# Performance work log

Measured on AMD Instinct MI355X. Metric: run time of the kernel, lower is better.

## Reference

```python
import jax, jax.numpy as jnp
import numpy as np

N, T, D, H = 100000, 16, 8, 40
HP1 = H + 1
ALPHA_DP = 1.0
KAPPA0 = 1000.0   # priorGaussianVarKappa
NU0 = 100.0       # priorWishartNu
PSI0_SCALE = 500.0  # priorWishartPsi = 500*I


def setup_inputs() -> dict:
    key = jax.random.key(0)
    ks = jax.random.split(key, 6)
    return {
        "BetaGamma1": jnp.ones((1, T), jnp.float32),
        "Phi": jax.random.uniform(ks[0], (N, T), jnp.float32),
        "inputData": jax.random.normal(ks[1], (N, D), jnp.float32),
        "outputData": jax.random.normal(ks[2], (N, 1), jnp.float32),
        "weightELM": jax.random.uniform(ks[3], (D, H), jnp.float32) * 2.0 - 1.0,
        "biasELM": jax.random.normal(ks[4], (H, 1), jnp.float32),
        "epsilonA": jnp.ones((1, T), jnp.float32),
        "epsilonB": jnp.ones((1, T), jnp.float32),
        "zetaA": 1e-4 * jnp.ones((1, T), jnp.float32),
        "zetaB": jnp.ones((1, T), jnp.float32),
    }


def reference(BetaGamma1, Phi, inputData, outputData, weightELM, biasELM,
              epsilonA, epsilonB, zetaA, zetaB):
    f32 = jnp.float32
    mu0 = jnp.zeros((D, 1), f32)                      # priorGaussianMeanMu
    Psi0 = PSI0_SCALE * jnp.eye(D, dtype=f32)         # priorWishartPsi

    sumPhi = jnp.sum(Phi, axis=0, keepdims=True)      # [1,T]

    # stick-breaking Beta params. Torch builds a flipped [T,N,T] tril mask;
    # mathematically BetaGamma2[t] = alpha + sum_{j>t} sum_n Phi[n,j]
    BetaGamma1_new = jnp.ones_like(BetaGamma1) + sumPhi
    col = sumPhi[0]                                   # [T]
    rev_incl = jnp.cumsum(col[::-1])[::-1]            # sum_{j>=t}
    BetaGamma2 = (ALPHA_DP + (rev_incl - col))[None, :]

    # Gaussian-Wishart natural-parameter updates.
    # Torch loops over clusters doing [N,D,D] bmm outer products; this is
    # S[:,:,t] = sum_n Phi[n,t] x_n x_n^T
    S = jnp.einsum('nt,ni,nj->ijt', Phi, inputData, inputData)  # [D,D,T]
    t11 = -0.5 * (Psi0 + KAPPA0 * mu0 @ mu0.T)[:, :, None] - 0.5 * S
    t12 = KAPPA0 * mu0 + inputData.T @ Phi            # [D,T]
    t21 = -0.5 * sumPhi - 0.5 * (NU0 + D + 2)         # [1,T]
    kappa = KAPPA0 + sumPhi                           # [1,T]
    mu = t12 / kappa                                  # [D,T]
    nu = -2.0 * t21 - 2.0 - float(D)                  # [1,T]
    psi = -2.0 * t11 - kappa[0][None, None, :] * jnp.einsum('it,jt->ijt', mu, mu)

    # ELM feature map + augmented design matrix X = [sigmoid(x W + b), 1]
    hmap = jax.nn.sigmoid(inputData @ weightELM + biasELM.T)   # [N,H]
    X = jnp.concatenate([hmap, jnp.ones((inputData.shape[0], 1), f32)], axis=1)  # [N,HP1]

    epsExp = (epsilonA / epsilonB)[0]                 # [T]
    zetaExp = (zetaA / zetaB)[0]                      # [T]

    # A[t] = X^T diag(Phi[:,t]) X   (torch: per-cluster bmm with diag_embed)
    A = jnp.einsum('nt,ni,nj->tij', Phi, X, X)        # [T,HP1,HP1]
    WS = jnp.linalg.inv(epsExp[:, None, None] * A
                        + zetaExp[:, None, None] * jnp.eye(HP1, dtype=f32))
    # b[t] = X^T diag(Phi[:,t]) y
    b = jnp.einsum('ni,nt->ti', X * outputData, Phi)  # [T,HP1]
    WMv = zetaExp[:, None] * jnp.einsum('tij,tj->ti', WS, b)   # [T,HP1]
    WM = WMv[:, :, None]                              # [T,HP1,1]

    # prior Zeta/Epsilon alias the variational initial values in __init__
    zetaA_new = zetaA + (H + 1) * 0.5
    zetaB_new = zetaB + 0.5 * (jnp.sum(WMv * WMv, axis=1)
                               + jnp.trace(WS, axis1=-2, axis2=-1))[None, :]
    epsA_new = epsilonA + 0.5 * sumPhi

    pred = jnp.einsum('ni,ti->tn', X, WMv)            # [T,N]
    err = outputData.T - pred                          # [T,N]
    t1 = jnp.einsum('tn,nt->t', err * err, Phi)[None, :]
    t2 = jnp.einsum('tij,tji->t', A, WS)[None, :]
    epsB_new = epsilonB + 0.5 * (t1 + t2)

    return (BetaGamma1_new, BetaGamma2, mu, kappa, nu, psi,
            WM, WS, zetaA_new, zetaB_new, epsA_new, epsB_new)
```

## Files before the change

kernel.cpp:

```cpp
#include <hip/hip_runtime.h>

#define Nn 100000
#define Tt 16
#define Dd 8
#define Hh 40
#define HP1 41

#define SPC 13
#define CH  (32 * SPC)
#define KCMAX ((Nn + CH - 1) / CH)

#define CSZ 53248
#define XEH_OFF  0
#define XEL_OFF  (XEH_OFF + 32 * Nn)
#define PHIT_OFF (XEL_OFF + 32 * Nn)
#define PART_OFF (PHIT_OFF + 16 * Nn)
#define P_OFF    (PART_OFF + 8 * CSZ)

#define OFF_BG1   0
#define OFF_BG2   16
#define OFF_MU    32
#define OFF_KAPPA 160
#define OFF_NU    176
#define OFF_PSI   192
#define OFF_WM    1216
#define OFF_WS    1872
#define OFF_ZA    28768
#define OFF_ZB    28784
#define OFF_EA    28800
#define OFF_EB    28816

typedef _Float16 f16x8 __attribute__((ext_vector_type(8)));
typedef float f32x4 __attribute__((ext_vector_type(4)));
typedef unsigned int u32x4 __attribute__((ext_vector_type(4)));

#define AIDX(i, t, j) ((((i) * 16 + (t)) * 64) + (j))

__global__ __launch_bounds__(256)
void elm_expand(const float* __restrict__ Phi, const float* __restrict__ Xd,
                const float* __restrict__ Yd, const float* __restrict__ W,
                const float* __restrict__ bb,
                unsigned short* __restrict__ XeHi, unsigned short* __restrict__ XeLo,
                float* __restrict__ PhiT)
{
  __shared__ float sW[Dd * Hh];
  __shared__ float sb[Hh];
  __shared__ float xs[64][9];
  __shared__ float ys[64];
  __shared__ float hrow[64][41];
  __shared__ float pt[16][68];
  int tid = threadIdx.x;
  int n0 = blockIdx.x * 64;

  for (int i = tid; i < Dd * Hh; i += 256) sW[i] = W[i];
  if (tid < Hh) sb[tid] = bb[tid];
  if (tid < 128) {
    int nl = tid >> 1, h4 = (tid & 1) * 4;
    int gn = n0 + nl;
    float4 v = (gn < Nn) ? *(const float4*)(Xd + (size_t)gn * 8 + h4)
                         : make_float4(0.f, 0.f, 0.f, 0.f);
    xs[nl][h4 + 0] = v.x; xs[nl][h4 + 1] = v.y;
    xs[nl][h4 + 2] = v.z; xs[nl][h4 + 3] = v.w;
  }
  if (tid < 64) { int gn = n0 + tid; ys[tid] = (gn < Nn) ? Yd[gn] : 0.f; }
  {
    int nl = tid >> 2, q = tid & 3;
    int gn = n0 + nl;
    float4 v = (gn < Nn) ? *(const float4*)(Phi + (size_t)gn * 16 + q * 4)
                         : make_float4(0.f, 0.f, 0.f, 0.f);
    pt[q * 4 + 0][nl] = v.x; pt[q * 4 + 1][nl] = v.y;
    pt[q * 4 + 2][nl] = v.z; pt[q * 4 + 3][nl] = v.w;
  }
  __syncthreads();
  {
    int nl = tid >> 2, hq = (tid & 3) * 10;
    for (int hh = 0; hh < 10; ++hh) {
      int h = hq + hh;
      float z = sb[h];
#pragma unroll
      for (int d = 0; d < 8; ++d) z = fmaf(xs[nl][d], sW[d * Hh + h], z);
      hrow[nl][h] = 1.f / (1.f + __expf(-z));
    }
  }
  __syncthreads();
  {
    int t = tid & 15, nq = tid >> 4;
    int gn = n0 + nq * 4;
    if (gn < Nn) {
      float4 v = make_float4(pt[t][nq * 4 + 0], pt[t][nq * 4 + 1],
                             pt[t][nq * 4 + 2], pt[t][nq * 4 + 3]);
      *(float4*)(PhiT + (size_t)t * Nn + gn) = v;
    }
  }
  {
    int cidx = tid >> 2, seg = tid & 3;
    int nl0 = seg * 16;
    float vv[16];
#pragma unroll
    for (int j = 0; j < 16; ++j) {
      int n = nl0 + j;
      float v;
      if (cidx < Hh) v = hrow[n][cidx];
      else if (cidx == 40) v = 1.f;
      else if (cidx < 49) v = xs[n][cidx - 41];
      else if (cidx == 49) v = ys[n];
      else v = 0.f;
      vv[j] = v;
    }
    unsigned short hs[16], ls[16];
#pragma unroll
    for (int j = 0; j < 16; ++j) {
      _Float16 h = (_Float16)vv[j];
      float r = vv[j] - (float)h;
      _Float16 lo = (_Float16)r;
      hs[j] = __builtin_bit_cast(unsigned short, h);
      ls[j] = __builtin_bit_cast(unsigned short, lo);
    }
#pragma unroll
    for (int q2 = 0; q2 < 2; ++q2) {
      int gn = n0 + nl0 + q2 * 8;
      if (gn < Nn) {
        uint4 uh, ul;
        uh.x = hs[q2*8+0] | ((unsigned)hs[q2*8+1] << 16);
        uh.y = hs[q2*8+2] | ((unsigned)hs[q2*8+3] << 16);
        uh.z = hs[q2*8+4] | ((unsigned)hs[q2*8+5] << 16);
        uh.w = hs[q2*8+6] | ((unsigned)hs[q2*8+7] << 16);
        ul.x = ls[q2*8+0] | ((unsigned)ls[q2*8+1] << 16);
        ul.y = ls[q2*8+2] | ((unsigned)ls[q2*8+3] << 16);
        ul.z = ls[q2*8+4] | ((unsigned)ls[q2*8+5] << 16);
        ul.w = ls[q2*8+6] | ((unsigned)ls[q2*8+7] << 16);
        *(uint4*)(XeHi + (size_t)cidx * Nn + gn) = uh;
        *(uint4*)(XeLo + (size_t)cidx * Nn + gn) = ul;
      }
    }
  }
}

__device__ __forceinline__ void gload16(const void* g, void* l) {
  __builtin_amdgcn_global_load_lds(
      (const __attribute__((address_space(1))) unsigned int*)g,
      (__attribute__((address_space(3))) unsigned int*)l, 16, 0, 0);
}

#define PHI_LDS 32768
#define LDS_BYTES (PHI_LDS + 16 * CH * 4)

__global__ __launch_bounds__(512, 2)
void gram_mfma(const float* __restrict__ PhiT,
               const unsigned short* __restrict__ XeHi,
               const unsigned short* __restrict__ XeLo,
               float* __restrict__ P)
{
  __shared__ __align__(16) char smem[LDS_BYTES];

  int tid = threadIdx.x;
  int l = tid & 63, w = tid >> 6;
  int l15 = l & 15, lg = l >> 4;

  int MT  = (w < 4) ? 7 : 6;
  int i0w = (w < 4) ? 7 * w : 28 + 6 * (w - 4);

  int off_b[4];
#pragma unroll
  for (int nt = 0; nt < 4; ++nt) {
    int j = l15 + 16 * nt;
    off_b[nt] = j * 64 + 16 * (lg ^ (j & 3));
  }
  int off_a[7];
#pragma unroll
  for (int mi = 0; mi < 7; ++mi) {
    int i = i0w + mi;
    off_a[mi] = i * 64 + 16 * (lg ^ (i & 3));
  }
  int off_p0 = l15 * 128 + 16 * ((2 * lg) ^ (l15 & 7));
  int off_p1 = l15 * 128 + 16 * ((2 * lg + 1) ^ (l15 & 7));
  int ld0 = tid * 16;
  int brow = (tid & 255) >> 2, bsl = tid & 3;
  const unsigned short* bplane = (tid < 256) ? XeHi : XeLo;

  f32x4 acc[7][4];
#pragma unroll
  for (int mi = 0; mi < 7; ++mi)
#pragma unroll
    for (int nt = 0; nt < 4; ++nt) acc[mi][nt] = (f32x4){0.f, 0.f, 0.f, 0.f};

  for (int cc = blockIdx.x; cc < KCMAX; cc += gridDim.x) {
    int n0 = cc * CH;
    int rem = Nn - n0; if (rem > CH) rem = CH;
    int nsteps = rem >> 5;

    __builtin_amdgcn_s_barrier();
    asm volatile("" ::: "memory");

    const char* gB = (const char*)(bplane + (size_t)brow * Nn + n0
                                   + 8 * (bsl ^ (brow & 3)));
#define STAGE(sx) gload16(gB + (size_t)(sx) * 64, \
                          &smem[(((sx) & 3) * 8192) + ld0])

#pragma unroll
    for (int q = 0; q < 4; ++q) {
      int gp = tid + q * 512;
      if (gp < 16 * CH / 4) {
        int s = gp >> 7, qq = gp & 127, t = qq >> 3, sl = qq & 7;
        gload16(PhiT + (size_t)t * Nn + n0 + s * 32 + 4 * (sl ^ (t & 7)),
                &smem[PHI_LDS + gp * 16]);
      }
    }
    STAGE(0);
    if (nsteps > 1) STAGE(1);
    if (nsteps > 2) STAGE(2);

    for (int s = 0; s < nsteps; ++s) {
      int out = nsteps - 1 - s; if (out > 2) out = 2;
      if (out == 2)      asm volatile("s_waitcnt vmcnt(2)" ::: "memory");
      else if (out == 1) asm volatile("s_waitcnt vmcnt(1)" ::: "memory");
      else               asm volatile("s_waitcnt vmcnt(0)" ::: "memory");
      __builtin_amdgcn_s_barrier();
      asm volatile("" ::: "memory");
      if (s + 3 < nsteps) STAGE(s + 3);

      const char* base  = &smem[(s & 3) * 8192];
      const char* pbase = &smem[PHI_LDS + s * 2048];
      f32x4 p0 = *(const f32x4*)(pbase + off_p0);
      f32x4 p1 = *(const f32x4*)(pbase + off_p1);
      float ph[8] = {p0[0], p0[1], p0[2], p0[3], p1[0], p1[1], p1[2], p1[3]};

      f16x8 bh[4], bl[4];
#pragma unroll
      for (int nt = 0; nt < 4; ++nt) {
        bh[nt] = *(const f16x8*)(base + off_b[nt]);
        bl[nt] = *(const f16x8*)(base + 4096 + off_b[nt]);
      }
      __builtin_amdgcn_s_setprio(1);
#pragma unroll
      for (int mi = 0; mi < 7; ++mi) {
        if (mi >= MT) break;
        f16x8 xh = *(const f16x8*)(base + off_a[mi]);
        f16x8 xl = *(const f16x8*)(base + 4096 + off_a[mi]);
        float v0 = ph[0] * ((float)xh[0] + (float)xl[0]);
        float v1 = ph[1] * ((float)xh[1] + (float)xl[1]);
        float v2 = ph[2] * ((float)xh[2] + (float)xl[2]);
        float v3 = ph[3] * ((float)xh[3] + (float)xl[3]);
        float v4 = ph[4] * ((float)xh[4] + (float)xl[4]);
        float v5 = ph[5] * ((float)xh[5] + (float)xl[5]);
        float v6 = ph[6] * ((float)xh[6] + (float)xl[6]);
        float v7 = ph[7] * ((float)xh[7] + (float)xl[7]);
        auto h0 = __builtin_amdgcn_cvt_pkrtz(v0, v1);
        auto h1 = __builtin_amdgcn_cvt_pkrtz(v2, v3);
        auto h2 = __builtin_amdgcn_cvt_pkrtz(v4, v5);
        auto h3 = __builtin_amdgcn_cvt_pkrtz(v6, v7);
        float r0 = v0 - (float)h0[0], r1 = v1 - (float)h0[1];
        float r2 = v2 - (float)h1[0], r3 = v3 - (float)h1[1];
        float r4 = v4 - (float)h2[0], r5 = v5 - (float)h2[1];
        float r6 = v6 - (float)h3[0], r7 = v7 - (float)h3[1];
        auto e0 = __builtin_amdgcn_cvt_pkrtz(r0, r1);
        auto e1 = __builtin_amdgcn_cvt_pkrtz(r2, r3);
        auto e2 = __builtin_amdgcn_cvt_pkrtz(r4, r5);
        auto e3 = __builtin_amdgcn_cvt_pkrtz(r6, r7);
        u32x4 uh = {__builtin_bit_cast(unsigned int, h0), __builtin_bit_cast(unsigned int, h1),
                    __builtin_bit_cast(unsigned int, h2), __builtin_bit_cast(unsigned int, h3)};
        u32x4 ul = {__builtin_bit_cast(unsigned int, e0), __builtin_bit_cast(unsigned int, e1),
                    __builtin_bit_cast(unsigned int, e2), __builtin_bit_cast(unsigned int, e3)};
        f16x8 ah = __builtin_bit_cast(f16x8, uh);
        f16x8 al = __builtin_bit_cast(f16x8, ul);
#pragma unroll
        for (int nt = 0; nt < 4; ++nt) {
          acc[mi][nt] = __builtin_amdgcn_mfma_f32_16x16x32_f16(ah, bh[nt], acc[mi][nt], 0, 0, 0);
          acc[mi][nt] = __builtin_amdgcn_mfma_f32_16x16x32_f16(ah, bl[nt], acc[mi][nt], 0, 0, 0);
          acc[mi][nt] = __builtin_amdgcn_mfma_f32_16x16x32_f16(al, bh[nt], acc[mi][nt], 0, 0, 0);
        }
      }
      __builtin_amdgcn_s_setprio(0);
    }
#undef STAGE
  }

  float* Pc = P + (size_t)blockIdx.x * CSZ;
#pragma unroll
  for (int mi = 0; mi < 7; ++mi) {
    if (mi >= MT) break;
    int i = i0w + mi;
#pragma unroll
    for (int nt = 0; nt < 4; ++nt) {
      int j = nt * 16 + l15;
#pragma unroll
      for (int r = 0; r < 4; ++r)
        Pc[(i * 16 + lg * 4 + r) * 64 + j] = acc[mi][nt][r];
    }
  }
}

__global__ __launch_bounds__(256)
void reduce_a(const float4* __restrict__ P4, int nslabs, float4* __restrict__ part4)
{
  int g = blockIdx.y;
  int idx = blockIdx.x * 256 + threadIdx.x;
  int per = (nslabs + 7) / 8;
  int c0 = g * per, c1 = c0 + per; if (c1 > nslabs) c1 = nslabs;
  float4 s = make_float4(0.f, 0.f, 0.f, 0.f);
  for (int cc = c0; cc < c1; ++cc) {
    float4 v = P4[(size_t)cc * (CSZ / 4) + idx];
    s.x += v.x; s.y += v.y; s.z += v.z; s.w += v.w;
  }
  part4[(size_t)g * (CSZ / 4) + idx] = s;
}

__device__ __forceinline__ float accv(const float* __restrict__ part, int idx) {
  float s = 0.f;
#pragma unroll
  for (int g = 0; g < 8; ++g) s += part[g * CSZ + idx];
  return s;
}

__global__ __launch_bounds__(256)
void finalize_kernel(const float* __restrict__ part, const float* __restrict__ epsA,
                     const float* __restrict__ epsB, const float* __restrict__ zetA,
                     const float* __restrict__ zetB, float* __restrict__ out)
{
  int t = blockIdx.x;
  int tid = threadIdx.x;
  __shared__ float G[HP1][84];
  __shared__ float As[HP1][HP1 + 1];
  __shared__ float bs[HP1];
  __shared__ float colk[HP1];
  __shared__ float red[256];
  __shared__ float wmv[HP1];
  __shared__ float rowv[4][HP1 + 1];
  __shared__ float mus[Dd];

  float epsExp = epsA[t] / epsB[t];
  float zetaExp = zetA[t] / zetB[t];

  for (int idx = tid; idx < HP1 * HP1; idx += 256) {
    int i = idx / HP1, j = idx % HP1;
    float a = accv(part, AIDX(i, t, j));
    As[i][j] = a;
    G[i][j] = epsExp * a + (i == j ? zetaExp : 0.f);
    G[i][41 + j] = (i == j) ? 1.f : 0.f;
  }
  for (int idx = tid; idx < HP1; idx += 256) {
    G[idx][82] = 0.f; G[idx][83] = 0.f;
    bs[idx] = accv(part, AIDX(idx, t, 49));
  }
  __syncthreads();

  int c = tid % HP1;
  int ig = tid / HP1;
  int irow0 = ig * 7;

  for (int k = 0; k < HP1; ++k) {
    float pivinv = 1.f / G[k][k];
    if (tid >= 1 && tid <= HP1) G[k][k + tid] *= pivinv;
    if (tid < HP1) colk[tid] = (tid == k) ? 0.f : G[tid][k];
    __syncthreads();
    if (ig < 6) {
      int j = k + 1 + c;
      float pk = G[k][j];
#pragma unroll
      for (int r = 0; r < 7; ++r) {
        int i = irow0 + r;
        if (i < HP1 && i != k) G[i][j] = fmaf(-colk[i], pk, G[i][j]);
      }
    }
    __syncthreads();
  }

  for (int idx = tid; idx < HP1 * HP1; idx += 256) {
    int i = idx / HP1, j = idx % HP1;
    out[OFF_WS + (t * HP1 + i) * HP1 + j] = G[i][41 + j];
  }
  if (tid < HP1) {
    float s = 0.f;
    for (int j = 0; j < HP1; ++j) s += G[tid][41 + j] * bs[j];
    float w = zetaExp * s;
    wmv[tid] = w;
    out[OFF_WM + t * HP1 + tid] = w;
  }
  __syncthreads();
  float lt2 = 0.f;
  for (int idx = tid; idx < HP1 * HP1; idx += 256) {
    int i = idx / HP1, j = idx % HP1;
    lt2 += As[i][j] * G[i][41 + j];
  }
  red[tid] = lt2; __syncthreads();
  for (int s = 128; s > 0; s >>= 1) {
    if (tid < s) red[tid] += red[tid + s];
    __syncthreads();
  }
  float t2v = red[0];
  if (tid < HP1) {
    float w = wmv[tid];
    float aw = 0.f;
    for (int j = 0; j < HP1; ++j) aw += As[tid][j] * wmv[j];
    rowv[0][tid] = w * bs[tid];
    rowv[1][tid] = w * w;
    rowv[2][tid] = G[tid][41 + tid];
    rowv[3][tid] = w * aw;
  }
  __syncthreads();

  float sp = accv(part, AIDX(40, t, 40));
  float kap = 1000.f + sp;
  float syy = accv(part, AIDX(49, t, 49));

  if (tid == 0) {
    float wb = 0.f, wn = 0.f, trc = 0.f, quad = 0.f;
    for (int i = 0; i < HP1; ++i) {
      wb += rowv[0][i]; wn += rowv[1][i]; trc += rowv[2][i]; quad += rowv[3][i];
    }
    float t1 = syy - 2.f * wb + quad;
    out[OFF_BG1 + t] = 1.f + sp;
    float rest = 0.f;
    for (int u = t + 1; u < Tt; ++u) rest += accv(part, AIDX(40, u, 40));
    out[OFF_BG2 + t] = 1.f + rest;
    out[OFF_KAPPA + t] = kap;
    out[OFF_NU + t] = sp + 100.f;
    out[OFF_ZA + t] = zetA[t] + 0.5f * (float)HP1;
    out[OFF_ZB + t] = zetB[t] + 0.5f * (wn + trc);
    out[OFF_EA + t] = epsA[t] + 0.5f * sp;
    out[OFF_EB + t] = epsB[t] + 0.5f * (t1 + t2v);
  }
  if (tid < Dd) {
    float m = accv(part, AIDX(40, t, 41 + tid)) / kap;
    mus[tid] = m;
    out[OFF_MU + tid * Tt + t] = m;
  }
  __syncthreads();
  if (tid < Dd * Dd) {
    int i = tid / Dd, j = tid % Dd;
    float S = accv(part, AIDX(41 + i, t, 41 + j));
    float v = (i == j ? 500.f : 0.f) + S - kap * mus[i] * mus[j];
    out[OFF_PSI + (i * Dd + j) * Tt + t] = v;
  }
}

extern "C" void kernel_launch(void* const* d_in, const int* in_sizes, int n_in,
                              void* d_out, int out_size, void* d_ws, size_t ws_size,
                              hipStream_t stream) {
  const float* Phi = (const float*)d_in[1];
  const float* Xd  = (const float*)d_in[2];
  const float* Yd  = (const float*)d_in[3];
  const float* W   = (const float*)d_in[4];
  const float* bb  = (const float*)d_in[5];
  const float* eA  = (const float*)d_in[6];
  const float* eB  = (const float*)d_in[7];
  const float* zA  = (const float*)d_in[8];
  const float* zB  = (const float*)d_in[9];
  float* out = (float*)d_out;
  float* ws  = (float*)d_ws;

  unsigned short* XeHi = (unsigned short*)(ws + XEH_OFF);
  unsigned short* XeLo = (unsigned short*)(ws + XEL_OFF);
  float* PhiT = ws + PHIT_OFF;
  float* part = ws + PART_OFF;
  float* P    = ws + P_OFF;

  long maxSlabs = ((long)(ws_size / 4) - (long)P_OFF) / CSZ;
  int grid1 = (int)(maxSlabs < KCMAX ? maxSlabs : KCMAX);
  if (grid1 < 1) grid1 = 1;

  hipLaunchKernelGGL(elm_expand, dim3((Nn + 63) / 64), dim3(256), 0, stream,
                     Phi, Xd, Yd, W, bb, XeHi, XeLo, PhiT);
  hipLaunchKernelGGL(gram_mfma, dim3(grid1), dim3(512), 0, stream,
                     PhiT, XeHi, XeLo, P);
  hipLaunchKernelGGL(reduce_a, dim3(52, 8), dim3(256), 0, stream,
                     (const float4*)P, grid1, (float4*)part);
  hipLaunchKernelGGL(finalize_kernel, dim3(Tt), dim3(256), 0, stream,
                     part, eA, eB, zA, zB, out);
}
```

Baseline: 170.5 us.

## Store packed upper-triangular Gram partials and shrink per-block chunk size

Per-block Gram partials are now stored only for the upper triangle of the 50x50 symmetric matrix, with the 16 clusters packed contiguously per pair. This shrinks each partial slab from 53248 to 20400 floats, cutting the global write and reduction traffic, and the reduce grid shrinks to match. The per-block chunk drops from 13 to 8 steps, so the gram kernel runs more blocks, and the Phi staging loop loses its bounds check. Finalize indexes through a packed triangle mapping, and smaller chunks mean more slabs to reduce.

```diff
diff --git a/kernel.cpp b/kernel.cpp
--- a/kernel.cpp
+++ b/kernel.cpp
@@ -6,16 +6,18 @@
 #define Hh 40
 #define HP1 41
 
-#define SPC 13
+#define SPC 8
 #define CH  (32 * SPC)
 #define KCMAX ((Nn + CH - 1) / CH)
 
-#define CSZ 53248
+#define NPAIR 1275
+#define PSZ (NPAIR * 16)
+
 #define XEH_OFF  0
 #define XEL_OFF  (XEH_OFF + 32 * Nn)
 #define PHIT_OFF (XEL_OFF + 32 * Nn)
 #define PART_OFF (PHIT_OFF + 16 * Nn)
-#define P_OFF    (PART_OFF + 8 * CSZ)
+#define P_OFF    (PART_OFF + 8 * PSZ)
 
 #define OFF_BG1   0
 #define OFF_BG2   16
@@ -34,7 +36,10 @@
 typedef float f32x4 __attribute__((ext_vector_type(4)));
 typedef unsigned int u32x4 __attribute__((ext_vector_type(4)));
 
-#define AIDX(i, t, j) ((((i) * 16 + (t)) * 64) + (j))
+__device__ __forceinline__ int pidx(int i, int j) {
+  if (i > j) { int tmp = i; i = j; j = tmp; }
+  return (i * (2 * 50 - i + 1)) / 2 + (j - i);
+}
 
 __global__ __launch_bounds__(256)
 void elm_expand(const float* __restrict__ Phi, const float* __restrict__ Xd,
@@ -198,13 +203,11 @@
                           &smem[(((sx) & 3) * 8192) + ld0])
 
 #pragma unroll
-    for (int q = 0; q < 4; ++q) {
+    for (int q = 0; q < 2; ++q) {
       int gp = tid + q * 512;
-      if (gp < 16 * CH / 4) {
-        int s = gp >> 7, qq = gp & 127, t = qq >> 3, sl = qq & 7;
-        gload16(PhiT + (size_t)t * Nn + n0 + s * 32 + 4 * (sl ^ (t & 7)),
-                &smem[PHI_LDS + gp * 16]);
-      }
+      int s = gp >> 7, qq = gp & 127, t = qq >> 3, sl = qq & 7;
+      gload16(PhiT + (size_t)t * Nn + n0 + s * 32 + 4 * (sl ^ (t & 7)),
+              &smem[PHI_LDS + gp * 16]);
     }
     STAGE(0);
     if (nsteps > 1) STAGE(1);
@@ -275,17 +278,20 @@
 #undef STAGE
   }
 
-  float* Pc = P + (size_t)blockIdx.x * CSZ;
+  float* Pc = P + (size_t)blockIdx.x * PSZ;
 #pragma unroll
   for (int mi = 0; mi < 7; ++mi) {
     if (mi >= MT) break;
     int i = i0w + mi;
-#pragma unroll
-    for (int nt = 0; nt < 4; ++nt) {
-      int j = nt * 16 + l15;
-#pragma unroll
-      for (int r = 0; r < 4; ++r)
-        Pc[(i * 16 + lg * 4 + r) * 64 + j] = acc[mi][nt][r];
+    if (i < 50) {
+#pragma unroll
+      for (int nt = 0; nt < 4; ++nt) {
+        int j = nt * 16 + l15;
+        if (j >= i && j < 50) {
+          int pb = (i * (101 - i)) / 2 + (j - i);
+          *(f32x4*)(Pc + pb * 16 + lg * 4) = acc[mi][nt];
+        }
+      }
     }
   }
 }
@@ -295,20 +301,21 @@
 {
   int g = blockIdx.y;
   int idx = blockIdx.x * 256 + threadIdx.x;
+  if (idx >= PSZ / 4) return;
   int per = (nslabs + 7) / 8;
   int c0 = g * per, c1 = c0 + per; if (c1 > nslabs) c1 = nslabs;
   float4 s = make_float4(0.f, 0.f, 0.f, 0.f);
   for (int cc = c0; cc < c1; ++cc) {
-    float4 v = P4[(size_t)cc * (CSZ / 4) + idx];
+    float4 v = P4[(size_t)cc * (PSZ / 4) + idx];
     s.x += v.x; s.y += v.y; s.z += v.z; s.w += v.w;
   }
-  part4[(size_t)g * (CSZ / 4) + idx] = s;
+  part4[(size_t)g * (PSZ / 4) + idx] = s;
 }
 
 __device__ __forceinline__ float accv(const float* __restrict__ part, int idx) {
   float s = 0.f;
 #pragma unroll
-  for (int g = 0; g < 8; ++g) s += part[g * CSZ + idx];
+  for (int g = 0; g < 8; ++g) s += part[g * PSZ + idx];
   return s;
 }
 
@@ -333,14 +340,14 @@
 
   for (int idx = tid; idx < HP1 * HP1; idx += 256) {
     int i = idx / HP1, j = idx % HP1;
-    float a = accv(part, AIDX(i, t, j));
+    float a = accv(part, pidx(i, j) * Tt + t);
     As[i][j] = a;
     G[i][j] = epsExp * a + (i == j ? zetaExp : 0.f);
     G[i][41 + j] = (i == j) ? 1.f : 0.f;
   }
   for (int idx = tid; idx < HP1; idx += 256) {
     G[idx][82] = 0.f; G[idx][83] = 0.f;
-    bs[idx] = accv(part, AIDX(idx, t, 49));
+    bs[idx] = accv(part, pidx(idx, 49) * Tt + t);
   }
   __syncthreads();
 
@@ -399,9 +406,9 @@
   }
   __syncthreads();
 
-  float sp = accv(part, AIDX(40, t, 40));
+  float sp = accv(part, pidx(40, 40) * Tt + t);
   float kap = 1000.f + sp;
-  float syy = accv(part, AIDX(49, t, 49));
+  float syy = accv(part, pidx(49, 49) * Tt + t);
 
   if (tid == 0) {
     float wb = 0.f, wn = 0.f, trc = 0.f, quad = 0.f;
@@ -411,7 +418,7 @@
     float t1 = syy - 2.f * wb + quad;
     out[OFF_BG1 + t] = 1.f + sp;
     float rest = 0.f;
-    for (int u = t + 1; u < Tt; ++u) rest += accv(part, AIDX(40, u, 40));
+    for (int u = t + 1; u < Tt; ++u) rest += accv(part, pidx(40, 40) * Tt + u);
     out[OFF_BG2 + t] = 1.f + rest;
     out[OFF_KAPPA + t] = kap;
     out[OFF_NU + t] = sp + 100.f;
@@ -421,14 +428,14 @@
     out[OFF_EB + t] = epsB[t] + 0.5f * (t1 + t2v);
   }
   if (tid < Dd) {
-    float m = accv(part, AIDX(40, t, 41 + tid)) / kap;
+    float m = accv(part, pidx(40, 41 + tid) * Tt + t) / kap;
     mus[tid] = m;
     out[OFF_MU + tid * Tt + t] = m;
   }
   __syncthreads();
   if (tid < Dd * Dd) {
     int i = tid / Dd, j = tid % Dd;
-    float S = accv(part, AIDX(41 + i, t, 41 + j));
+    float S = accv(part, pidx(41 + i, 41 + j) * Tt + t);
     float v = (i == j ? 500.f : 0.f) + S - kap * mus[i] * mus[j];
     out[OFF_PSI + (i * Dd + j) * Tt + t] = v;
   }
@@ -455,7 +462,7 @@
   float* part = ws + PART_OFF;
   float* P    = ws + P_OFF;
 
-  long maxSlabs = ((long)(ws_size / 4) - (long)P_OFF) / CSZ;
+  long maxSlabs = ((long)(ws_size / 4) - (long)P_OFF) / PSZ;
   int grid1 = (int)(maxSlabs < KCMAX ? maxSlabs : KCMAX);
   if (grid1 < 1) grid1 = 1;
 
@@ -463,7 +470,7 @@
                      Phi, Xd, Yd, W, bb, XeHi, XeLo, PhiT);
   hipLaunchKernelGGL(gram_mfma, dim3(grid1), dim3(512), 0, stream,
                      PhiT, XeHi, XeLo, P);
-  hipLaunchKernelGGL(reduce_a, dim3(52, 8), dim3(256), 0, stream,
+  hipLaunchKernelGGL(reduce_a, dim3(20, 8), dim3(256), 0, stream,
                      (const float4*)P, grid1, (float4*)part);
   hipLaunchKernelGGL(finalize_kernel, dim3(Tt), dim3(256), 0, stream,
                      part, eA, eB, zA, zB, out);
```

Result: slower. 188.0 us (+10.3%).
